# Kernel tuning notes

Measured on AMD Instinct MI355X. Metric: run time of the kernel, lower is better.

The kernel has to match this reference:

```python
import jax, jax.numpy as jnp
import numpy as np

N, E, L, H, C, F, NCLASS, NGRAPH = 50000, 800000, 3, 2, 64, 128, 10, 64
NEG_SLOPE = 0.2


def setup_inputs() -> dict:
    key = jax.random.key(0)
    ks = jax.random.split(key, 8)
    x = jax.random.normal(ks[0], (N, F), dtype=jnp.float32)
    edge_index = jax.random.randint(ks[1], (2, E), 0, N, dtype=jnp.int64)
    batch = jnp.sort(jax.random.randint(ks[2], (N,), 0, NGRAPH, dtype=jnp.int64))
    s = 1.0 / np.sqrt(F)
    W = jax.random.normal(ks[3], (L, F, H * C), dtype=jnp.float32) * s
    att_src = jax.random.normal(ks[4], (L, H, C), dtype=jnp.float32) * s
    att_dst = jax.random.normal(ks[5], (L, H, C), dtype=jnp.float32) * s
    bias = jnp.zeros((L, H * C), dtype=jnp.float32)
    lin_w = jax.random.normal(ks[6], (H * C, NCLASS), dtype=jnp.float32) * s
    lin_b = jnp.zeros((NCLASS,), dtype=jnp.float32)
    return {"x": x, "edge_index": edge_index, "batch": batch, "W": W,
            "att_src": att_src, "att_dst": att_dst, "bias": bias,
            "lin_w": lin_w, "lin_b": lin_b}


def _gat_layer(x, src, dst, w, a_s, a_d, b):
    n = x.shape[0]
    h = (x @ w).reshape(n, H, C)                      # [N,H,C]
    alpha_src = jnp.sum(h * a_s, axis=-1)             # [N,H]
    alpha_dst = jnp.sum(h * a_d, axis=-1)             # [N,H]
    e = jax.nn.leaky_relu(alpha_src[src] + alpha_dst[dst], NEG_SLOPE)  # [E2,H]
    # scatter-softmax over incoming edges of each destination node
    m = jax.ops.segment_max(e, dst, num_segments=n)
    p = jnp.exp(e - m[dst])
    z = jax.ops.segment_sum(p, dst, num_segments=n)
    alpha = p / z[dst]                                # [E2,H]
    msg = h[src] * alpha[:, :, None]                  # [E2,H,C]
    out = jax.ops.segment_sum(msg, dst, num_segments=n)  # [N,H,C]
    return out.reshape(n, H * C) + b


def reference(x, edge_index, batch, W, att_src, att_dst, bias, lin_w, lin_b):
    n = x.shape[0]
    # PyG GATConv default: add self-loops
    loop = jnp.arange(n, dtype=edge_index.dtype)
    src = jnp.concatenate([edge_index[0], loop])
    dst = jnp.concatenate([edge_index[1], loop])
    for l in range(L):
        x = _gat_layer(x, src, dst, W[l], att_src[l], att_dst[l], bias[l])
        x = jax.nn.elu(x)  # activation; dropout/bn inactive (eval, use_bn=False)
    # global mean pool per graph
    sums = jax.ops.segment_sum(x, batch, num_segments=NGRAPH)
    cnt = jax.ops.segment_sum(jnp.ones((n,), x.dtype), batch, num_segments=NGRAPH)
    pooled = sums / jnp.maximum(cnt, 1.0)[:, None]    # [NGRAPH, H*C]
    logits = pooled @ lin_w + lin_b
    return jax.nn.softmax(logits, axis=1)
```

## Files before the change

### kernel.cpp

```cpp
#include <hip/hip_runtime.h>
#include <math.h>

#define NNODES 50000
#define NEDGES 800000
#define NLAYERS 3
#define NHEADS 2
#define NCH 64
#define FDIM 128
#define NCLS 10
#define NGRAPH 64
#define NEG_SLOPE 0.2f
#define GEMMB ((NNODES + 63) / 64)
#define NB 391
#define RADB 391
#define PCH 8

#define WAVE_SYNC()                      \
  do {                                   \
    __builtin_amdgcn_wave_barrier();     \
    __asm__ volatile("" ::: "memory");   \
  } while (0)

typedef __attribute__((ext_vector_type(8))) short bf16x8;
typedef __attribute__((ext_vector_type(4))) float f32x4;

__device__ __forceinline__ unsigned short f2bf(float f) {
  unsigned int u = __builtin_bit_cast(unsigned int, f);
  unsigned int r = u + 0x7FFFu + ((u >> 16) & 1u);
  return (unsigned short)(r >> 16);
}
__device__ __forceinline__ float bflo(unsigned v) {
  return __builtin_bit_cast(float, v << 16);
}
__device__ __forceinline__ float bfhi(unsigned v) {
  return __builtin_bit_cast(float, v & 0xFFFF0000u);
}

__global__ __launch_bounds__(256) void k_wprep(const float* __restrict__ W,
                                               unsigned* __restrict__ Wt,
                                               const int* __restrict__ batch,
                                               int* __restrict__ goff,
                                               float* __restrict__ gsum,
                                               int* __restrict__ bcnt) {
  __shared__ float Lt[128][132];
  int l = blockIdx.x;
  int t = threadIdx.x;
  if (l == NLAYERS) {
    if (t < NGRAPH) {
      int lo = 0, hi = NNODES;
      while (lo < hi) {
        int mid = (lo + hi) >> 1;
        if (batch[mid] < t) lo = mid + 1;
        else hi = mid;
      }
      goff[t] = lo;
    }
    if (t == 0) goff[NGRAPH] = NNODES;
    for (int i = t; i < NGRAPH * FDIM; i += 256) gsum[i] = 0.f;
    for (int i = t; i < NB; i += 256) bcnt[i] = 0;
    return;
  }
  const float* Wl = W + (size_t)l * FDIM * FDIM;
  unsigned* Wtl = Wt + (size_t)l * FDIM * FDIM / 2;
#pragma unroll
  for (int i = 0; i < 16; ++i) {
    int k = (t >> 5) + 8 * i;
    int n4 = (t & 31) * 4;
    float4 v = *(const float4*)(Wl + (size_t)k * 128 + n4);
    Lt[k][n4 + 0] = v.x;
    Lt[k][n4 + 1] = v.y;
    Lt[k][n4 + 2] = v.z;
    Lt[k][n4 + 3] = v.w;
  }
  __syncthreads();
  int n = t >> 1;
  int kh = (t & 1) * 64;
  for (int kk = 0; kk < 64; kk += 2) {
    unsigned pk = (unsigned)f2bf(Lt[kh + kk][n]) |
                  ((unsigned)f2bf(Lt[kh + kk + 1][n]) << 16);
    Wtl[n * 64 + (kh >> 1) + (kk >> 1)] = pk;
  }
}

template <bool BF16IN>
__device__ __forceinline__ void gemm_body(int blk, const void* __restrict__ Xv,
                                          const unsigned* __restrict__ Wt,
                                          const float* __restrict__ a_sL,
                                          const float* __restrict__ a_dL,
                                          unsigned* __restrict__ Hb,
                                          float* __restrict__ as_,
                                          float* __restrict__ ad_) {
  int t = threadIdx.x;
  int lane = t & 63;
  int w = t >> 6;
  int row0 = blk * 64;
  int n16 = lane & 15;
  int quad = lane >> 4;
  int m0 = w * 16;

  int gr = row0 + m0 + n16;
  size_t rbase = (size_t)min(gr, NNODES - 1) * 128;

  f32x4 acc[8];
#pragma unroll
  for (int nt = 0; nt < 8; ++nt) {
    f32x4 z = {0.f, 0.f, 0.f, 0.f};
    acc[nt] = z;
  }
#pragma unroll
  for (int kk = 0; kk < 4; ++kk) {
    bf16x8 af;
    if constexpr (BF16IN) {
      const unsigned short* xp = (const unsigned short*)Xv + rbase;
      af = *(const bf16x8*)(xp + kk * 32 + quad * 8);
    } else {
      const float* xp = (const float*)Xv + rbase;
      float4 va = *(const float4*)(xp + kk * 32 + quad * 8);
      float4 vb = *(const float4*)(xp + kk * 32 + quad * 8 + 4);
      af[0] = (short)f2bf(va.x); af[1] = (short)f2bf(va.y);
      af[2] = (short)f2bf(va.z); af[3] = (short)f2bf(va.w);
      af[4] = (short)f2bf(vb.x); af[5] = (short)f2bf(vb.y);
      af[6] = (short)f2bf(vb.z); af[7] = (short)f2bf(vb.w);
    }
#pragma unroll
    for (int nt = 0; nt < 8; ++nt) {
      bf16x8 bf = *(const bf16x8*)(Wt + (size_t)(nt * 16 + n16) * 64 +
                                   kk * 16 + quad * 4);
      acc[nt] =
          __builtin_amdgcn_mfma_f32_16x16x32_bf16(af, bf, acc[nt], 0, 0, 0);
    }
  }

  float asv[8], adv[8];
#pragma unroll
  for (int nt = 0; nt < 8; ++nt) {
    asv[nt] = a_sL[nt * 16 + n16];
    adv[nt] = a_dL[nt * 16 + n16];
  }
#pragma unroll
  for (int r = 0; r < 4; ++r) {
    int row = row0 + m0 + quad * 4 + r;
    bool ok = (row < NNODES);
    float ps0 = 0.f, pd0 = 0.f, ps1 = 0.f, pd1 = 0.f;
#pragma unroll
    for (int nt = 0; nt < 4; ++nt) {
      ps0 += acc[nt][r] * asv[nt];
      pd0 += acc[nt][r] * adv[nt];
      ps1 += acc[nt + 4][r] * asv[nt + 4];
      pd1 += acc[nt + 4][r] * adv[nt + 4];
    }
#pragma unroll
    for (int off = 1; off < 16; off <<= 1) {
      ps0 += __shfl_xor(ps0, off, 64);
      pd0 += __shfl_xor(pd0, off, 64);
      ps1 += __shfl_xor(ps1, off, 64);
      pd1 += __shfl_xor(pd1, off, 64);
    }
    if (ok && n16 == 0) {
      as_[row * 2 + 0] = ps0;
      as_[row * 2 + 1] = ps1;
      ad_[row * 2 + 0] = pd0;
      ad_[row * 2 + 1] = pd1;
    }
    if (ok) {
#pragma unroll
      for (int nt = 0; nt < 4; ++nt) {
        unsigned pk = (unsigned)f2bf(acc[nt][r]) |
                      ((unsigned)f2bf(acc[nt + 4][r]) << 16);
        Hb[(size_t)row * 64 + nt * 16 + n16] = pk;
      }
    }
  }
}

__global__ __launch_bounds__(256) void k_gemm(
    const unsigned short* __restrict__ Xh, const unsigned* __restrict__ Wt,
    const float* __restrict__ a_sL, const float* __restrict__ a_dL,
    unsigned* __restrict__ Hb, float* __restrict__ as_,
    float* __restrict__ ad_) {
  gemm_body<true>(blockIdx.x, Xh, Wt, a_sL, a_dL, Hb, as_, ad_);
}

__global__ __launch_bounds__(256) void k_front(
    const float* __restrict__ X, const unsigned* __restrict__ Wt,
    const float* __restrict__ a_sL, const float* __restrict__ a_dL,
    unsigned* __restrict__ Hb, float* __restrict__ as_,
    float* __restrict__ ad_, const int* __restrict__ ei, int* __restrict__ bh,
    int* __restrict__ bcnt) {
  int b = blockIdx.x;
  if (b < GEMMB) {
    gemm_body<false>(b, X, Wt, a_sL, a_dL, Hb, as_, ad_);
  } else {
    __shared__ int hist[NB];
    int blk = b - GEMMB;
    int t = threadIdx.x;
    for (int i = t; i < NB; i += 256) hist[i] = 0;
    __syncthreads();
    int e0 = blk * 2048;
#pragma unroll
    for (int i = 0; i < 8; ++i) {
      int e = e0 + i * 256 + t;
      if (e < NEDGES) atomicAdd(&hist[ei[NEDGES + e] >> 7], 1);
    }
    __syncthreads();
    for (int i = t; i < NB; i += 256) {
      int c = hist[i];
      int base = c ? atomicAdd(&bcnt[i], c) : 0;
      bh[i * RADB + blk] = base;
    }
  }
}

__global__ __launch_bounds__(256) void k_bscan(const int* __restrict__ bcnt,
                                               int* __restrict__ bstart) {
  __shared__ int ps[256];
  int t = threadIdx.x;
  int x0 = (2 * t < NB) ? bcnt[2 * t] : 0;
  int x1 = (2 * t + 1 < NB) ? bcnt[2 * t + 1] : 0;
  int pair = x0 + x1;
  ps[t] = pair;
  __syncthreads();
  for (int off = 1; off < 256; off <<= 1) {
    int v = (t >= off) ? ps[t - off] : 0;
    __syncthreads();
    ps[t] += v;
    __syncthreads();
  }
  int ex = ps[t] - pair;
  if (2 * t < NB) bstart[2 * t] = ex;
  if (2 * t + 1 < NB) bstart[2 * t + 1] = ex + x0;
  if (t == 0) bstart[NB] = NEDGES;
}

__global__ __launch_bounds__(256) void k_passB(const int* __restrict__ ei,
                                               const int* __restrict__ bstart,
                                               const int* __restrict__ bh,
                                               unsigned* __restrict__ ebuf) {
  __shared__ int curs[NB];
  int blk = blockIdx.x, t = threadIdx.x;
  for (int i = t; i < NB; i += 256) curs[i] = bstart[i] + bh[i * RADB + blk];
  __syncthreads();
  int e0 = blk * 2048;
#pragma unroll
  for (int i = 0; i < 8; ++i) {
    int e = e0 + i * 256 + t;
    if (e < NEDGES) {
      int s = ei[e];
      int d = ei[NEDGES + e];
      int pos = atomicAdd(&curs[d >> 7], 1);
      ebuf[pos] = ((unsigned)s << 7) | (unsigned)(d & 127);
    }
  }
}

__global__ __launch_bounds__(256) void k_passC(const unsigned* __restrict__ ebuf,
                                               const int* __restrict__ bstart,
                                               int* __restrict__ row_ptr,
                                               int* __restrict__ csr) {
  __shared__ int deg[128];
  __shared__ int scn[128];
  int b = blockIdx.x, t = threadIdx.x;
  int node0 = b * 128;
  int nn = min(128, NNODES - node0);
  int estart = bstart[b];
  int eend = bstart[b + 1];
  if (t < 128) deg[t] = 0;
  __syncthreads();
  for (int e = estart + t; e < eend; e += 256)
    atomicAdd(&deg[ebuf[e] & 127], 1);
  __syncthreads();
  if (t < 128) scn[t] = (t < nn) ? deg[t] + 1 : 0;
  __syncthreads();
  for (int off = 1; off < 128; off <<= 1) {
    int v = (t < 128 && t >= off) ? scn[t - off] : 0;
    __syncthreads();
    if (t < 128) scn[t] += v;
    __syncthreads();
  }
  int base = estart + node0;
  if (t < nn) {
    int st = base + (t ? scn[t - 1] : 0);
    row_ptr[node0 + t] = st;
    csr[st] = node0 + t;
    deg[t] = st + 1;
  }
  if (b == 0 && t == 0) row_ptr[NNODES] = NEDGES + NNODES;
  __syncthreads();
  for (int e = estart + t; e < eend; e += 256) {
    unsigned v = ebuf[e];
    int pos = atomicAdd(&deg[v & 127], 1);
    csr[pos] = (int)(v >> 7);
  }
}

__global__ __launch_bounds__(256) void k_aggregate(
    const unsigned* __restrict__ Hb, const float* __restrict__ as_,
    const float* __restrict__ ad_, const int* __restrict__ row_ptr,
    const int* __restrict__ csr, const float* __restrict__ bias,
    float* __restrict__ Xout, unsigned short* __restrict__ XoutH) {
  __shared__ float2 wb[4][64];
  __shared__ int sb[4][64];
  int wv = threadIdx.x >> 6;
  int lane = threadIdx.x & 63;
  int node = blockIdx.x * 4 + wv;
  if (node >= NNODES) return;
  int rs = row_ptr[node], re = row_ptr[node + 1];
  float2 adv = *(const float2*)&ad_[node * 2];
  const unsigned* Hl = Hb + lane;

  float z0 = 0.f, z1 = 0.f, acc0 = 0.f, acc1 = 0.f;
  for (int base = rs; base < re; base += 64) {
    int j = base + lane;
    int s = 0;
    if (j < re) s = csr[j];
    sb[wv][lane] = s;
    WAVE_SYNC();
    unsigned va[8];
#pragma unroll
    for (int u = 0; u < 8; ++u) va[u] = Hl[(size_t)sb[wv][u] * 64];
    float p0 = 0.f, p1 = 0.f;
    if (j < re) {
      float2 asv = *(const float2*)&as_[s * 2];
      float e0 = asv.x + adv.x; e0 = (e0 > 0.f) ? e0 : NEG_SLOPE * e0;
      float e1 = asv.y + adv.y; e1 = (e1 > 0.f) ? e1 : NEG_SLOPE * e1;
      p0 = __expf(e0);
      p1 = __expf(e1);
    }
    z0 += p0;
    z1 += p1;
    wb[wv][lane] = make_float2(p0, p1);
    WAVE_SYNC();
    int cl = min(64, re - base);
    int cl8 = (cl + 7) & ~7;
    int jj = 8;
    for (; jj < cl8; jj += 8) {
      unsigned vb2[8];
#pragma unroll
      for (int u = 0; u < 8; ++u) vb2[u] = Hl[(size_t)sb[wv][jj + u] * 64];
#pragma unroll
      for (int u = 0; u < 8; ++u) {
        float2 w = wb[wv][jj - 8 + u];
        acc0 += w.x * bflo(va[u]);
        acc1 += w.y * bfhi(va[u]);
      }
#pragma unroll
      for (int u = 0; u < 8; ++u) va[u] = vb2[u];
    }
#pragma unroll
    for (int u = 0; u < 8; ++u) {
      float2 w = wb[wv][jj - 8 + u];
      acc0 += w.x * bflo(va[u]);
      acc1 += w.y * bfhi(va[u]);
    }
    WAVE_SYNC();
  }
#pragma unroll
  for (int off = 32; off > 0; off >>= 1) {
    z0 += __shfl_xor(z0, off, 64);
    z1 += __shfl_xor(z1, off, 64);
  }
  float o0 = acc0 / z0 + bias[lane];
  float o1 = acc1 / z1 + bias[64 + lane];
  o0 = (o0 > 0.f) ? o0 : expm1f(o0);
  o1 = (o1 > 0.f) ? o1 : expm1f(o1);
  if (XoutH) {
    XoutH[(size_t)node * 128 + lane] = f2bf(o0);
    XoutH[(size_t)node * 128 + 64 + lane] = f2bf(o1);
  } else {
    Xout[(size_t)node * 128 + lane] = o0;
    Xout[(size_t)node * 128 + 64 + lane] = o1;
  }
}

__global__ __launch_bounds__(256) void k_pool2(const float* __restrict__ Xf,
                                               const int* __restrict__ goff,
                                               float* __restrict__ gsum) {
  __shared__ float red[128];
  int b = blockIdx.x;
  int g = b >> 3, ch = b & 7;
  int t = threadIdx.x;
  int c = t & 127, rh = t >> 7;
  int s = goff[g], e = goff[g + 1];
  int len = e - s;
  int c0 = s + (len * ch) / PCH;
  int c1 = s + (len * (ch + 1)) / PCH;
  float acc = 0.f;
  for (int n = c0 + rh; n < c1; n += 2) acc += Xf[(size_t)n * 128 + c];
  if (rh) red[c] = acc;
  __syncthreads();
  if (!rh) atomicAdd(&gsum[g * FDIM + c], acc + red[c]);
}

__global__ __launch_bounds__(64) void k_final(const float* __restrict__ gsum,
                                              const int* __restrict__ goff,
                                              const float* __restrict__ lw,
                                              const float* __restrict__ lb,
                                              float* __restrict__ out) {
  int g = threadIdx.x;
  float cnt = (float)(goff[g + 1] - goff[g]);
  float inv = 1.f / fmaxf(cnt, 1.f);
  float lg[NCLS];
#pragma unroll
  for (int k = 0; k < NCLS; ++k) lg[k] = lb[k];
  for (int c = 0; c < FDIM; ++c) {
    float pv = gsum[g * FDIM + c] * inv;
#pragma unroll
    for (int k = 0; k < NCLS; ++k) lg[k] += pv * lw[c * NCLS + k];
  }
  float mx = lg[0];
#pragma unroll
  for (int k = 1; k < NCLS; ++k) mx = fmaxf(mx, lg[k]);
  float s = 0.f;
#pragma unroll
  for (int k = 0; k < NCLS; ++k) {
    lg[k] = expf(lg[k] - mx);
    s += lg[k];
  }
  float invs = 1.f / s;
#pragma unroll
  for (int k = 0; k < NCLS; ++k) out[g * NCLS + k] = lg[k] * invs;
}


extern "C" void kernel_launch(void* const* d_in, const int* in_sizes, int n_in,
                              void* d_out, int out_size, void* d_ws,
                              size_t ws_size, hipStream_t stream) {
  const float* x = (const float*)d_in[0];
  const int* ei = (const int*)d_in[1];
  const int* batch = (const int*)d_in[2];
  const float* W = (const float*)d_in[3];
  const float* a_s = (const float*)d_in[4];
  const float* a_d = (const float*)d_in[5];
  const float* bias = (const float*)d_in[6];
  const float* lw = (const float*)d_in[7];
  const float* lb = (const float*)d_in[8];
  float* out = (float*)d_out;

  unsigned* Hb = (unsigned*)d_ws;
  float* xb = (float*)(Hb + (size_t)NNODES * 64);
  float* as_ = xb + (size_t)NNODES * 128;
  float* ad_ = as_ + (size_t)NNODES * 2;
  float* gsum = ad_ + (size_t)NNODES * 2;
  int* goff = (int*)(gsum + NGRAPH * FDIM);
  int* bcnt = goff + (NGRAPH + 1);
  int* bstart = bcnt + NB;
  int* row_ptr = bstart + (NB + 1);
  int* csr = row_ptr + (NNODES + 1);
  int* bh = csr + (NEDGES + NNODES);
  unsigned* ebuf = (unsigned*)(bh + NB * RADB);
  unsigned* Wt = ebuf + (NEDGES + 1024);
  unsigned short* xbh = (unsigned short*)(Wt + 3 * 8192);

  k_wprep<<<NLAYERS + 1, 256, 0, stream>>>(W, Wt, batch, goff, gsum, bcnt);
  k_front<<<GEMMB + RADB, 256, 0, stream>>>(x, Wt, a_s, a_d, Hb, as_, ad_, ei,
                                            bh, bcnt);
  k_bscan<<<1, 256, 0, stream>>>(bcnt, bstart);
  k_passB<<<RADB, 256, 0, stream>>>(ei, bstart, bh, ebuf);
  k_passC<<<NB, 256, 0, stream>>>(ebuf, bstart, row_ptr, csr);

  for (int l = 0; l < NLAYERS; ++l) {
    if (l > 0) {
      k_gemm<<<GEMMB, 256, 0, stream>>>(xbh, Wt + (size_t)l * FDIM * FDIM / 2,
                                        a_s + l * FDIM, a_d + l * FDIM, Hb,
                                        as_, ad_);
    }
    unsigned short* oh = (l < NLAYERS - 1) ? xbh : nullptr;
    k_aggregate<<<(NNODES + 3) / 4, 256, 0, stream>>>(
        Hb, as_, ad_, row_ptr, csr, bias + l * FDIM, xb, oh);
  }
  k_pool2<<<NGRAPH * PCH, 256, 0, stream>>>(xb, goff, gsum);
  k_final<<<1, 64, 0, stream>>>(gsum, goff, lw, lb, out);
}
```

Before: 312.0 us.

## Fold bucket scan into passB, fuse final softmax into pool, widen GEMM tiles

Three changes. The single-block bucket scan is now recomputed redundantly in every passB block, and the separate final classifier kernel is folded into the pool kernel using a last-block-done atomic counter. Together these remove two kernel launches and their serial gaps. The GEMM also now computes two 16-row M tiles per wave (128 rows per block), reusing each B fragment across both. This halves the GEMM block count but raises register pressure.

```diff
diff --git a/kernel.cpp b/kernel.cpp
--- a/kernel.cpp
+++ b/kernel.cpp
@@ -10,7 +10,7 @@
 #define NCLS 10
 #define NGRAPH 64
 #define NEG_SLOPE 0.2f
-#define GEMMB ((NNODES + 63) / 64)
+#define GEMMB ((NNODES + 127) / 128)
 #define NB 391
 #define RADB 391
 #define PCH 8
@@ -41,7 +41,8 @@
                                                const int* __restrict__ batch,
                                                int* __restrict__ goff,
                                                float* __restrict__ gsum,
-                                               int* __restrict__ bcnt) {
+                                               int* __restrict__ bcnt,
+                                               int* __restrict__ done) {
   __shared__ float Lt[128][132];
   int l = blockIdx.x;
   int t = threadIdx.x;
@@ -55,7 +56,10 @@
       }
       goff[t] = lo;
     }
-    if (t == 0) goff[NGRAPH] = NNODES;
+    if (t == 0) {
+      goff[NGRAPH] = NNODES;
+      *done = 0;
+    }
     for (int i = t; i < NGRAPH * FDIM; i += 256) gsum[i] = 0.f;
     for (int i = t; i < NB; i += 256) bcnt[i] = 0;
     return;
@@ -93,41 +97,48 @@
   int t = threadIdx.x;
   int lane = t & 63;
   int w = t >> 6;
-  int row0 = blk * 64;
   int n16 = lane & 15;
   int quad = lane >> 4;
-  int m0 = w * 16;
-
-  int gr = row0 + m0 + n16;
-  size_t rbase = (size_t)min(gr, NNODES - 1) * 128;
-
-  f32x4 acc[8];
-#pragma unroll
-  for (int nt = 0; nt < 8; ++nt) {
-    f32x4 z = {0.f, 0.f, 0.f, 0.f};
-    acc[nt] = z;
-  }
+  int rowb = blk * 128 + w * 32;
+
+  size_t rb[2];
+  rb[0] = (size_t)min(rowb + n16, NNODES - 1) * 128;
+  rb[1] = (size_t)min(rowb + 16 + n16, NNODES - 1) * 128;
+
+  f32x4 acc[2][8];
+#pragma unroll
+  for (int mt = 0; mt < 2; ++mt)
+#pragma unroll
+    for (int nt = 0; nt < 8; ++nt) {
+      f32x4 z = {0.f, 0.f, 0.f, 0.f};
+      acc[mt][nt] = z;
+    }
 #pragma unroll
   for (int kk = 0; kk < 4; ++kk) {
-    bf16x8 af;
-    if constexpr (BF16IN) {
-      const unsigned short* xp = (const unsigned short*)Xv + rbase;
-      af = *(const bf16x8*)(xp + kk * 32 + quad * 8);
-    } else {
-      const float* xp = (const float*)Xv + rbase;
-      float4 va = *(const float4*)(xp + kk * 32 + quad * 8);
-      float4 vb = *(const float4*)(xp + kk * 32 + quad * 8 + 4);
-      af[0] = (short)f2bf(va.x); af[1] = (short)f2bf(va.y);
-      af[2] = (short)f2bf(va.z); af[3] = (short)f2bf(va.w);
-      af[4] = (short)f2bf(vb.x); af[5] = (short)f2bf(vb.y);
-      af[6] = (short)f2bf(vb.z); af[7] = (short)f2bf(vb.w);
+    bf16x8 af[2];
+#pragma unroll
+    for (int mt = 0; mt < 2; ++mt) {
+      if constexpr (BF16IN) {
+        const unsigned short* xp = (const unsigned short*)Xv + rb[mt];
+        af[mt] = *(const bf16x8*)(xp + kk * 32 + quad * 8);
+      } else {
+        const float* xp = (const float*)Xv + rb[mt];
+        float4 va = *(const float4*)(xp + kk * 32 + quad * 8);
+        float4 vb = *(const float4*)(xp + kk * 32 + quad * 8 + 4);
+        af[mt][0] = (short)f2bf(va.x); af[mt][1] = (short)f2bf(va.y);
+        af[mt][2] = (short)f2bf(va.z); af[mt][3] = (short)f2bf(va.w);
+        af[mt][4] = (short)f2bf(vb.x); af[mt][5] = (short)f2bf(vb.y);
+        af[mt][6] = (short)f2bf(vb.z); af[mt][7] = (short)f2bf(vb.w);
+      }
     }
 #pragma unroll
     for (int nt = 0; nt < 8; ++nt) {
       bf16x8 bf = *(const bf16x8*)(Wt + (size_t)(nt * 16 + n16) * 64 +
                                    kk * 16 + quad * 4);
-      acc[nt] =
-          __builtin_amdgcn_mfma_f32_16x16x32_bf16(af, bf, acc[nt], 0, 0, 0);
+      acc[0][nt] =
+          __builtin_amdgcn_mfma_f32_16x16x32_bf16(af[0], bf, acc[0][nt], 0, 0, 0);
+      acc[1][nt] =
+          __builtin_amdgcn_mfma_f32_16x16x32_bf16(af[1], bf, acc[1][nt], 0, 0, 0);
     }
   }
 
@@ -138,36 +149,39 @@
     adv[nt] = a_dL[nt * 16 + n16];
   }
 #pragma unroll
-  for (int r = 0; r < 4; ++r) {
-    int row = row0 + m0 + quad * 4 + r;
-    bool ok = (row < NNODES);
-    float ps0 = 0.f, pd0 = 0.f, ps1 = 0.f, pd1 = 0.f;
-#pragma unroll
-    for (int nt = 0; nt < 4; ++nt) {
-      ps0 += acc[nt][r] * asv[nt];
-      pd0 += acc[nt][r] * adv[nt];
-      ps1 += acc[nt + 4][r] * asv[nt + 4];
-      pd1 += acc[nt + 4][r] * adv[nt + 4];
-    }
-#pragma unroll
-    for (int off = 1; off < 16; off <<= 1) {
-      ps0 += __shfl_xor(ps0, off, 64);
-      pd0 += __shfl_xor(pd0, off, 64);
-      ps1 += __shfl_xor(ps1, off, 64);
-      pd1 += __shfl_xor(pd1, off, 64);
-    }
-    if (ok && n16 == 0) {
-      as_[row * 2 + 0] = ps0;
-      as_[row * 2 + 1] = ps1;
-      ad_[row * 2 + 0] = pd0;
-      ad_[row * 2 + 1] = pd1;
-    }
-    if (ok) {
+  for (int mt = 0; mt < 2; ++mt) {
+#pragma unroll
+    for (int r = 0; r < 4; ++r) {
+      int row = rowb + mt * 16 + quad * 4 + r;
+      bool ok = (row < NNODES);
+      float ps0 = 0.f, pd0 = 0.f, ps1 = 0.f, pd1 = 0.f;
 #pragma unroll
       for (int nt = 0; nt < 4; ++nt) {
-        unsigned pk = (unsigned)f2bf(acc[nt][r]) |
-                      ((unsigned)f2bf(acc[nt + 4][r]) << 16);
-        Hb[(size_t)row * 64 + nt * 16 + n16] = pk;
+        ps0 += acc[mt][nt][r] * asv[nt];
+        pd0 += acc[mt][nt][r] * adv[nt];
+        ps1 += acc[mt][nt + 4][r] * asv[nt + 4];
+        pd1 += acc[mt][nt + 4][r] * adv[nt + 4];
+      }
+#pragma unroll
+      for (int off = 1; off < 16; off <<= 1) {
+        ps0 += __shfl_xor(ps0, off, 64);
+        pd0 += __shfl_xor(pd0, off, 64);
+        ps1 += __shfl_xor(ps1, off, 64);
+        pd1 += __shfl_xor(pd1, off, 64);
+      }
+      if (ok && n16 == 0) {
+        as_[row * 2 + 0] = ps0;
+        as_[row * 2 + 1] = ps1;
+        ad_[row * 2 + 0] = pd0;
+        ad_[row * 2 + 1] = pd1;
+      }
+      if (ok) {
+#pragma unroll
+        for (int nt = 0; nt < 4; ++nt) {
+          unsigned pk = (unsigned)f2bf(acc[mt][nt][r]) |
+                        ((unsigned)f2bf(acc[mt][nt + 4][r]) << 16);
+          Hb[(size_t)row * 64 + nt * 16 + n16] = pk;
+        }
       }
     }
   }
@@ -211,10 +225,14 @@
   }
 }
 
-__global__ __launch_bounds__(256) void k_bscan(const int* __restrict__ bcnt,
+__global__ __launch_bounds__(256) void k_passB(const int* __restrict__ ei,
+                                               const int* __restrict__ bcnt,
+                                               const int* __restrict__ bh,
+                                               unsigned* __restrict__ ebuf,
                                                int* __restrict__ bstart) {
+  __shared__ int curs[NB];
   __shared__ int ps[256];
-  int t = threadIdx.x;
+  int blk = blockIdx.x, t = threadIdx.x;
   int x0 = (2 * t < NB) ? bcnt[2 * t] : 0;
   int x1 = (2 * t + 1 < NB) ? bcnt[2 * t + 1] : 0;
   int pair = x0 + x1;
@@ -227,18 +245,15 @@
     __syncthreads();
   }
   int ex = ps[t] - pair;
-  if (2 * t < NB) bstart[2 * t] = ex;
-  if (2 * t + 1 < NB) bstart[2 * t + 1] = ex + x0;
-  if (t == 0) bstart[NB] = NEDGES;
-}
-
-__global__ __launch_bounds__(256) void k_passB(const int* __restrict__ ei,
-                                               const int* __restrict__ bstart,
-                                               const int* __restrict__ bh,
-                                               unsigned* __restrict__ ebuf) {
-  __shared__ int curs[NB];
-  int blk = blockIdx.x, t = threadIdx.x;
-  for (int i = t; i < NB; i += 256) curs[i] = bstart[i] + bh[i * RADB + blk];
+  if (2 * t < NB) {
+    curs[2 * t] = ex + bh[(2 * t) * RADB + blk];
+    if (blk == 0) bstart[2 * t] = ex;
+  }
+  if (2 * t + 1 < NB) {
+    curs[2 * t + 1] = ex + x0 + bh[(2 * t + 1) * RADB + blk];
+    if (blk == 0) bstart[2 * t + 1] = ex + x0;
+  }
+  if (blk == 0 && t == 0) bstart[NB] = NEDGES;
   __syncthreads();
   int e0 = blk * 2048;
 #pragma unroll
@@ -374,8 +389,13 @@
 
 __global__ __launch_bounds__(256) void k_pool2(const float* __restrict__ Xf,
                                                const int* __restrict__ goff,
-                                               float* __restrict__ gsum) {
+                                               float* __restrict__ gsum,
+                                               int* __restrict__ done,
+                                               const float* __restrict__ lw,
+                                               const float* __restrict__ lb,
+                                               float* __restrict__ out) {
   __shared__ float red[128];
+  __shared__ int lastflag;
   int b = blockIdx.x;
   int g = b >> 3, ch = b & 7;
   int t = threadIdx.x;
@@ -389,36 +409,40 @@
   if (rh) red[c] = acc;
   __syncthreads();
   if (!rh) atomicAdd(&gsum[g * FDIM + c], acc + red[c]);
-}
-
-__global__ __launch_bounds__(64) void k_final(const float* __restrict__ gsum,
-                                              const int* __restrict__ goff,
-                                              const float* __restrict__ lw,
-                                              const float* __restrict__ lb,
-                                              float* __restrict__ out) {
-  int g = threadIdx.x;
-  float cnt = (float)(goff[g + 1] - goff[g]);
-  float inv = 1.f / fmaxf(cnt, 1.f);
-  float lg[NCLS];
-#pragma unroll
-  for (int k = 0; k < NCLS; ++k) lg[k] = lb[k];
-  for (int c = 0; c < FDIM; ++c) {
-    float pv = gsum[g * FDIM + c] * inv;
-#pragma unroll
-    for (int k = 0; k < NCLS; ++k) lg[k] += pv * lw[c * NCLS + k];
-  }
-  float mx = lg[0];
-#pragma unroll
-  for (int k = 1; k < NCLS; ++k) mx = fmaxf(mx, lg[k]);
-  float s = 0.f;
-#pragma unroll
-  for (int k = 0; k < NCLS; ++k) {
-    lg[k] = expf(lg[k] - mx);
-    s += lg[k];
-  }
-  float invs = 1.f / s;
-#pragma unroll
-  for (int k = 0; k < NCLS; ++k) out[g * NCLS + k] = lg[k] * invs;
+  __syncthreads();
+  if (t == 0) {
+    __threadfence();
+    int prev = atomicAdd(done, 1);
+    lastflag = (prev == NGRAPH * PCH - 1) ? 1 : 0;
+  }
+  __syncthreads();
+  if (!lastflag) return;
+  __threadfence();
+  if (t < NGRAPH) {
+    int g2 = t;
+    float cnt = (float)(goff[g2 + 1] - goff[g2]);
+    float inv = 1.f / fmaxf(cnt, 1.f);
+    float lg[NCLS];
+#pragma unroll
+    for (int k = 0; k < NCLS; ++k) lg[k] = lb[k];
+    for (int cc = 0; cc < FDIM; ++cc) {
+      float pv = gsum[g2 * FDIM + cc] * inv;
+#pragma unroll
+      for (int k = 0; k < NCLS; ++k) lg[k] += pv * lw[cc * NCLS + k];
+    }
+    float mx = lg[0];
+#pragma unroll
+    for (int k = 1; k < NCLS; ++k) mx = fmaxf(mx, lg[k]);
+    float ssum = 0.f;
+#pragma unroll
+    for (int k = 0; k < NCLS; ++k) {
+      lg[k] = expf(lg[k] - mx);
+      ssum += lg[k];
+    }
+    float invs = 1.f / ssum;
+#pragma unroll
+    for (int k = 0; k < NCLS; ++k) out[g2 * NCLS + k] = lg[k] * invs;
+  }
 }
 
 
@@ -450,12 +474,13 @@
   unsigned* ebuf = (unsigned*)(bh + NB * RADB);
   unsigned* Wt = ebuf + (NEDGES + 1024);
   unsigned short* xbh = (unsigned short*)(Wt + 3 * 8192);
-
-  k_wprep<<<NLAYERS + 1, 256, 0, stream>>>(W, Wt, batch, goff, gsum, bcnt);
+  int* done = (int*)(xbh + (size_t)NNODES * 128);
+
+  k_wprep<<<NLAYERS + 1, 256, 0, stream>>>(W, Wt, batch, goff, gsum, bcnt,
+                                           done);
   k_front<<<GEMMB + RADB, 256, 0, stream>>>(x, Wt, a_s, a_d, Hb, as_, ad_, ei,
                                             bh, bcnt);
-  k_bscan<<<1, 256, 0, stream>>>(bcnt, bstart);
-  k_passB<<<RADB, 256, 0, stream>>>(ei, bstart, bh, ebuf);
+  k_passB<<<RADB, 256, 0, stream>>>(ei, bcnt, bh, ebuf, bstart);
   k_passC<<<NB, 256, 0, stream>>>(ebuf, bstart, row_ptr, csr);
 
   for (int l = 0; l < NLAYERS; ++l) {
@@ -468,6 +493,5 @@
     k_aggregate<<<(NNODES + 3) / 4, 256, 0, stream>>>(
         Hb, as_, ad_, row_ptr, csr, bias + l * FDIM, xb, oh);
   }
-  k_pool2<<<NGRAPH * PCH, 256, 0, stream>>>(xb, goff, gsum);
-  k_final<<<1, 64, 0, stream>>>(gsum, goff, lw, lb, out);
-}
+  k_pool2<<<NGRAPH * PCH, 256, 0, stream>>>(xb, goff, gsum, done, lw, lb, out);
+}
```

New measurement: 299.9 us. 1.04x faster.
